# Optimization experiments

Hardware: AMD Instinct MI355X
Metric: run time of the kernel (lower is better)

Reference implementation:

```python
import jax, jax.numpy as jnp
import numpy as np

B, T, D = 2, 1024, 2048
H = 16
NOPE, ROPE = 128, 64
QKD = NOPE + ROPE          # 192
QLORA, KVLORA = 1536, 512
VHD = 128
INTER = 8192
EPS = 1e-6
# NOTE: faithful to source: softscale = qk_head_dim * -0.5 (a large negative
# multiplier, NOT qk_head_dim ** -0.5). We reproduce the exact math.
SOFTSCALE = QKD * -0.5


def rmsnorm(x, w):
    return x * jax.lax.rsqrt(jnp.mean(jnp.square(x), axis=-1, keepdims=True) + EPS) * w


def apply_rope(x, cos, sin):
    # x: [B, T, h, rd] with rd even; cos/sin: [T, rd//2]
    x2 = x.reshape(x.shape[:-1] + (-1, 2))
    x0, x1 = x2[..., 0], x2[..., 1]
    c = cos[None, :, None, :]
    s = sin[None, :, None, :]
    r0 = x0 * c - x1 * s
    r1 = x0 * s + x1 * c
    return jnp.stack([r0, r1], axis=-1).reshape(x.shape)


def setup_inputs() -> dict:
    key = jax.random.key(0)
    ks = jax.random.split(key, 12)

    def w(k, o, i):
        return jax.random.normal(k, (o, i), jnp.float32) * 0.02

    x = jax.random.normal(ks[0], (B, T, D), jnp.float32)
    # RoPE angle tables for the rope sub-dim
    inv_freq = 1.0 / (10000.0 ** (jnp.arange(0, ROPE, 2, dtype=jnp.float32) / ROPE))
    ang = jnp.arange(T, dtype=jnp.float32)[:, None] * inv_freq[None, :]  # [T, ROPE//2]
    # causal additive mask [T, T]
    mask = jnp.where(jnp.tril(jnp.ones((T, T), bool)), 0.0, -1e9).astype(jnp.float32)
    return {
        "x": x,
        "mask": mask,
        "freqs_cos": jnp.cos(ang),
        "freqs_sin": jnp.sin(ang),
        "attn_norm_w": jnp.ones((D,), jnp.float32),
        "wq_a": w(ks[1], QLORA, D),
        "q_norm_w": jnp.ones((QLORA,), jnp.float32),
        "wq_b": w(ks[2], H * QKD, QLORA),
        "wkv_a": w(ks[3], KVLORA + ROPE, D),
        "kv_norm_w": jnp.ones((KVLORA,), jnp.float32),
        "wkv_b": w(ks[4], H * (NOPE + VHD), KVLORA),
        "wo": w(ks[5], D, H * VHD),
        "ffn_norm_w": jnp.ones((D,), jnp.float32),
        "w1": w(ks[6], INTER, D),
        "w2": w(ks[7], D, INTER),
        "w3": w(ks[8], INTER, D),
    }


def reference(x, mask, freqs_cos, freqs_sin, attn_norm_w, wq_a, q_norm_w, wq_b,
              wkv_a, kv_norm_w, wkv_b, wo, ffn_norm_w, w1, w2, w3):
    b, t, d = x.shape
    # --- MLA attention sub-block (pre-norm + residual) ---
    h = rmsnorm(x, attn_norm_w)
    # low-rank query: wq_b(q_norm(wq_a(h)))
    q = rmsnorm(h @ wq_a.T, q_norm_w) @ wq_b.T          # [b, t, H*QKD]
    q = q.reshape(b, t, H, QKD)
    q_nope, q_pe = q[..., :NOPE], q[..., NOPE:]
    q_pe = apply_rope(q_pe, freqs_cos, freqs_sin)
    # low-rank kv + decoupled rope key
    kv_all = h @ wkv_a.T                                 # [b, t, KVLORA+ROPE]
    kv_lat, k_pe = kv_all[..., :KVLORA], kv_all[..., KVLORA:]
    k_pe = apply_rope(k_pe[:, :, None, :], freqs_cos, freqs_sin)  # [b, t, 1, ROPE]
    kv = rmsnorm(kv_lat, kv_norm_w) @ wkv_b.T            # [b, t, H*(NOPE+VHD)]
    kv = kv.reshape(b, t, H, NOPE + VHD)
    k_nope, v = kv[..., :NOPE], kv[..., NOPE:]
    qf = jnp.concatenate([q_nope, q_pe], axis=-1)        # [b, t, H, QKD]
    kf = jnp.concatenate([k_nope, jnp.broadcast_to(k_pe, (b, t, H, ROPE))], axis=-1)
    scores = jnp.einsum('bshd,bthd->bsht', qf, kf) * SOFTSCALE
    scores = scores + mask[:, None, :]                   # mask over (s, 1, t)
    attn = jax.nn.softmax(scores.astype(jnp.float32), axis=-1).astype(x.dtype)
    y = jnp.einsum('bsht,bthd->bshd', attn, v).reshape(b, t, H * VHD)
    x = x + y @ wo.T
    # --- MLP sub-block (pre-norm + residual), SwiGLU ---
    h2 = rmsnorm(x, ffn_norm_w)
    out = x + (jax.nn.silu(h2 @ w1.T) * (h2 @ w3.T)) @ w2.T
    return out
```

## Files before the change

kernel.cpp:

```cpp
#include <hip/hip_runtime.h>
#include <hip/hip_bf16.h>
#include <cstddef>


#define TT 1024
#define DD 2048
#define QBLK 64
#define KVB 32

using bf16 = __hip_bfloat16;
typedef __attribute__((ext_vector_type(8))) short short8;
typedef __attribute__((ext_vector_type(8))) unsigned short ushort8v;
typedef __attribute__((ext_vector_type(4))) float f32x4;

__device__ __forceinline__ float us2f(unsigned short u) {
    return __uint_as_float(((unsigned int)u) << 16);
}
__device__ __forceinline__ float ldf(const void* p, size_t i, int isbf) {
    return isbf ? us2f(((const unsigned short*)p)[i]) : ((const float*)p)[i];
}
__device__ __forceinline__ unsigned short f2bf(float f) {
    __hip_bfloat16 b = __float2bfloat16(f);
    return *reinterpret_cast<unsigned short*>(&b);
}

__global__ __launch_bounds__(64) void detect_k(const void* __restrict__ x,
                                               int* __restrict__ flag)
{
    __shared__ int cnt;
    if (threadIdx.x == 0) cnt = 0;
    __syncthreads();
    const unsigned short* u = (const unsigned short*)x;
    int bad = 0;
    for (int i = threadIdx.x; i < 512; i += 64) {
        const float v = us2f(u[i]);
        const float a = fabsf(v);
        if (!(a < 1e6f) || (v != 0.0f && a < 1e-30f)) bad++;
    }
    atomicAdd(&cnt, bad);
    __syncthreads();
    if (threadIdx.x == 0) *flag = (cnt > 32) ? 0 : 1;
}

__global__ __launch_bounds__(256) void cvt_bf_k(
    const void* __restrict__ src, unsigned short* __restrict__ dst,
    size_t n, const int* __restrict__ flag)
{
    const int isbf = *flag;
    const size_t stride = (size_t)gridDim.x * 2048;
    for (size_t i = ((size_t)blockIdx.x * 256 + threadIdx.x) * 8; i < n; i += stride) {
        if (isbf) {
            *(ushort8v*)(dst + i) = *(const ushort8v*)((const unsigned short*)src + i);
        } else {
            const float* s = (const float*)src + i;
            float4 f0 = *(const float4*)s, f1 = *(const float4*)(s + 4);
            unsigned short t[8] = {f2bf(f0.x), f2bf(f0.y), f2bf(f0.z), f2bf(f0.w),
                                   f2bf(f1.x), f2bf(f1.y), f2bf(f1.z), f2bf(f1.w)};
            *(ushort8v*)(dst + i) = *(const ushort8v*)t;
        }
    }
}

__global__ __launch_bounds__(256) void cvt_hl_k(
    const void* __restrict__ src, unsigned short* __restrict__ dh,
    unsigned short* __restrict__ dl, size_t n, const int* __restrict__ flag)
{
    const int isbf = *flag;
    const size_t stride = (size_t)gridDim.x * 2048;
    for (size_t i = ((size_t)blockIdx.x * 256 + threadIdx.x) * 8; i < n; i += stride) {
        unsigned short th[8], tl[8];
        if (isbf) {
            const unsigned short* s = (const unsigned short*)src + i;
#pragma unroll
            for (int u = 0; u < 8; ++u) { th[u] = s[u]; tl[u] = 0; }
        } else {
            const float* s = (const float*)src + i;
#pragma unroll
            for (int u = 0; u < 8; ++u) {
                const float v = s[u];
                th[u] = f2bf(v);
                tl[u] = f2bf(v - us2f(th[u]));
            }
        }
        *(ushort8v*)(dh + i) = *(const ushort8v*)th;
        *(ushort8v*)(dl + i) = *(const ushort8v*)tl;
    }
}

template <int S, int HASR>
__global__ __launch_bounds__(256) void combine_k(
    const float* __restrict__ p, const float* __restrict__ R,
    float* __restrict__ out, int n4)
{
    const int stride = gridDim.x * 256;
    const float4* pp = (const float4*)p;
    for (int i = blockIdx.x * 256 + threadIdx.x; i < n4; i += stride) {
        float4 o = pp[i];
#pragma unroll
        for (int s = 1; s < S; ++s) {
            const float4 b4 = pp[(size_t)s * n4 + i];
            o.x += b4.x; o.y += b4.y; o.z += b4.z; o.w += b4.w;
        }
        if (HASR) {
            const float4 r4 = ((const float4*)R)[i];
            o.x += r4.x; o.y += r4.y; o.z += r4.z; o.w += r4.w;
        }
        ((float4*)out)[i] = o;
    }
}

__global__ __launch_bounds__(256) void rmsnorm_hl_k(
    const float* __restrict__ in, const void* __restrict__ w,
    unsigned short* __restrict__ oh, unsigned short* __restrict__ ol,
    int L, int istride, const int* __restrict__ flag)
{
    const int isbf = *flag;
    const int m = blockIdx.x, tid = threadIdx.x;
    const float* row = in + (size_t)m * istride;
    float ss = 0.f;
    for (int i = tid; i < L; i += 256) { float v = row[i]; ss += v * v; }
    __shared__ float red[256];
    red[tid] = ss; __syncthreads();
    for (int s = 128; s > 0; s >>= 1) {
        if (tid < s) red[tid] += red[tid + s];
        __syncthreads();
    }
    const float scale = 1.0f / sqrtf(red[0] / (float)L + 1e-6f);
    unsigned short* hrow = oh + (size_t)m * L;
    unsigned short* lrow = ol + (size_t)m * L;
    for (int i = tid; i < L; i += 256) {
        const float v = row[i] * scale * ldf(w, i, isbf);
        const unsigned short hi = f2bf(v);
        hrow[i] = hi;
        lrow[i] = f2bf(v - us2f(hi));
    }
}

__global__ __launch_bounds__(256) void rmsnorm_bf_k(
    const float* __restrict__ in, const void* __restrict__ w,
    unsigned short* __restrict__ out, int L,
    const int* __restrict__ flag)
{
    const int isbf = *flag;
    const int m = blockIdx.x, tid = threadIdx.x;
    const float* row = in + (size_t)m * L;
    float ss = 0.f;
    for (int i = tid; i < L; i += 256) { float v = row[i]; ss += v * v; }
    __shared__ float red[256];
    red[tid] = ss; __syncthreads();
    for (int s = 128; s > 0; s >>= 1) {
        if (tid < s) red[tid] += red[tid + s];
        __syncthreads();
    }
    const float scale = 1.0f / sqrtf(red[0] / (float)L + 1e-6f);
    unsigned short* orow = out + (size_t)m * L;
    for (int i = tid; i < L; i += 256)
        orow[i] = f2bf(row[i] * scale * ldf(w, i, isbf));
}

__global__ __launch_bounds__(256) void rmsnorm_x_hl_k(
    const void* __restrict__ x, size_t eoff, const void* __restrict__ w,
    unsigned short* __restrict__ hh, unsigned short* __restrict__ hl,
    float* __restrict__ xf, const int* __restrict__ flag)
{
    const int isbf = *flag;
    const int m = blockIdx.x, tid = threadIdx.x;
    const size_t base = eoff + (size_t)m * DD;
    float* xrow = xf + (size_t)m * DD;
    float ss = 0.f;
    float vals[8];
    for (int i = 0; i < 8; ++i) {
        float v = ldf(x, base + tid + 256 * i, isbf);
        vals[i] = v; ss += v * v;
        xrow[tid + 256 * i] = v;
    }
    __shared__ float red[256];
    red[tid] = ss; __syncthreads();
    for (int s = 128; s > 0; s >>= 1) {
        if (tid < s) red[tid] += red[tid + s];
        __syncthreads();
    }
    const float scale = 1.0f / sqrtf(red[0] / (float)DD + 1e-6f);
    unsigned short* hrow = hh + (size_t)m * DD;
    unsigned short* lrow = hl + (size_t)m * DD;
    for (int i = 0; i < 8; ++i) {
        const float v = vals[i] * scale * ldf(w, tid + 256 * i, isbf);
        const unsigned short hi = f2bf(v);
        hrow[tid + 256 * i] = hi;
        lrow[tid + 256 * i] = f2bf(v - us2f(hi));
    }
}

__global__ __launch_bounds__(256) void gemm_mfma3_k(
    const unsigned short* __restrict__ Ah, const unsigned short* __restrict__ Al,
    const void* __restrict__ Wv, const unsigned short* __restrict__ Wlo,
    float* __restrict__ C, int N, int K, int klen,
    int presplit, const int* __restrict__ flag)
{
    __shared__ unsigned short Ash[128 * 40];
    __shared__ unsigned short Asl[128 * 40];
    __shared__ unsigned short Wsh[128 * 40];
    __shared__ unsigned short Wsl[128 * 40];
    const int tid = threadIdx.x;
    const int lane = tid & 63;
    const int wave = tid >> 6;
    const int wm = (wave >> 1) << 6, wn = (wave & 1) << 6;
    const int bm = blockIdx.y << 7, bn = blockIdx.x << 7;
    const int k0 = blockIdx.z * klen;
    const size_t zoff = (size_t)blockIdx.z * 1024 * N;
    const int srow = tid >> 1, scol = (tid & 1) << 4;
    const unsigned short* Ahld = Ah + (size_t)(bm + srow) * K + scol;
    const unsigned short* Alld = Al + (size_t)(bm + srow) * K + scol;
    const int wrow = bn + srow;
    const size_t wldbase = (size_t)((wrow < N) ? wrow : (N - 1)) * K + scol;
    unsigned short* Ahdst = &Ash[srow * 40 + scol];
    unsigned short* Aldst = &Asl[srow * 40 + scol];
    unsigned short* Whdst = &Wsh[srow * 40 + scol];
    unsigned short* Wldst = &Wsl[srow * 40 + scol];
    const int frow = lane & 15;
    const int fk = (lane >> 4) << 3;
    const int kend = k0 + klen;

    f32x4 acc[4][4] = {};

    if (presplit) {
        const unsigned short* Whp = (const unsigned short*)Wv + wldbase;
        const unsigned short* Wlp = Wlo + wldbase;
        ushort8v ca0h = *(const ushort8v*)(Ahld + k0);
        ushort8v ca1h = *(const ushort8v*)(Ahld + k0 + 8);
        ushort8v ca0l = *(const ushort8v*)(Alld + k0);
        ushort8v ca1l = *(const ushort8v*)(Alld + k0 + 8);
        ushort8v cw0h = *(const ushort8v*)(Whp + k0);
        ushort8v cw1h = *(const ushort8v*)(Whp + k0 + 8);
        ushort8v cw0l = *(const ushort8v*)(Wlp + k0);
        ushort8v cw1l = *(const ushort8v*)(Wlp + k0 + 8);
        for (int kt = k0; kt < kend; kt += 32) {
            __syncthreads();
            *(ushort8v*)Ahdst = ca0h; *(ushort8v*)(Ahdst + 8) = ca1h;
            *(ushort8v*)Aldst = ca0l; *(ushort8v*)(Aldst + 8) = ca1l;
            *(ushort8v*)Whdst = cw0h; *(ushort8v*)(Whdst + 8) = cw1h;
            *(ushort8v*)Wldst = cw0l; *(ushort8v*)(Wldst + 8) = cw1l;
            __syncthreads();
            const int nk = (kt + 32 < kend) ? kt + 32 : kt;
            ca0h = *(const ushort8v*)(Ahld + nk);
            ca1h = *(const ushort8v*)(Ahld + nk + 8);
            ca0l = *(const ushort8v*)(Alld + nk);
            ca1l = *(const ushort8v*)(Alld + nk + 8);
            cw0h = *(const ushort8v*)(Whp + nk);
            cw1h = *(const ushort8v*)(Whp + nk + 8);
            cw0l = *(const ushort8v*)(Wlp + nk);
            cw1l = *(const ushort8v*)(Wlp + nk + 8);

            short8 afh[4], afl[4], bfh[4], bfl[4];
#pragma unroll
            for (int i = 0; i < 4; ++i) {
                afh[i] = *(const short8*)&Ash[(wm + i * 16 + frow) * 40 + fk];
                afl[i] = *(const short8*)&Asl[(wm + i * 16 + frow) * 40 + fk];
            }
#pragma unroll
            for (int j = 0; j < 4; ++j) {
                bfh[j] = *(const short8*)&Wsh[(wn + j * 16 + frow) * 40 + fk];
                bfl[j] = *(const short8*)&Wsl[(wn + j * 16 + frow) * 40 + fk];
            }
#pragma unroll
            for (int i = 0; i < 4; ++i)
#pragma unroll
                for (int j = 0; j < 4; ++j) {
                    acc[i][j] = __builtin_amdgcn_mfma_f32_16x16x32_bf16(
                        afh[i], bfh[j], acc[i][j], 0, 0, 0);
                    acc[i][j] = __builtin_amdgcn_mfma_f32_16x16x32_bf16(
                        afh[i], bfl[j], acc[i][j], 0, 0, 0);
                    acc[i][j] = __builtin_amdgcn_mfma_f32_16x16x32_bf16(
                        afl[i], bfh[j], acc[i][j], 0, 0, 0);
                }
        }
    } else {
        const int isbf = *flag;
        for (int kt = k0; kt < kend; kt += 32) {
            ushort8v a0h = *(const ushort8v*)(Ahld + kt);
            ushort8v a1h = *(const ushort8v*)(Ahld + kt + 8);
            ushort8v a0l = *(const ushort8v*)(Alld + kt);
            ushort8v a1l = *(const ushort8v*)(Alld + kt + 8);
            ushort8v w0h, w1h, w0l, w1l;
            if (isbf) {
                const unsigned short* Wp = (const unsigned short*)Wv + wldbase + kt;
                w0h = *(const ushort8v*)(Wp);
                w1h = *(const ushort8v*)(Wp + 8);
                w0l = w0h ^ w0h;
                w1l = w0l;
            } else {
                const float* Wp = (const float*)Wv + wldbase + kt;
                unsigned short th[16], tl[16];
#pragma unroll
                for (int t4 = 0; t4 < 4; ++t4) {
                    float4 f = *(const float4*)(Wp + 4 * t4);
                    float fv[4] = {f.x, f.y, f.z, f.w};
#pragma unroll
                    for (int u = 0; u < 4; ++u) {
                        const unsigned short hi = f2bf(fv[u]);
                        th[4 * t4 + u] = hi;
                        tl[4 * t4 + u] = f2bf(fv[u] - us2f(hi));
                    }
                }
                w0h = *(ushort8v*)&th[0]; w1h = *(ushort8v*)&th[8];
                w0l = *(ushort8v*)&tl[0]; w1l = *(ushort8v*)&tl[8];
            }
            __syncthreads();
            *(ushort8v*)Ahdst = a0h; *(ushort8v*)(Ahdst + 8) = a1h;
            *(ushort8v*)Aldst = a0l; *(ushort8v*)(Aldst + 8) = a1l;
            *(ushort8v*)Whdst = w0h; *(ushort8v*)(Whdst + 8) = w1h;
            *(ushort8v*)Wldst = w0l; *(ushort8v*)(Wldst + 8) = w1l;
            __syncthreads();

            short8 afh[4], afl[4], bfh[4], bfl[4];
#pragma unroll
            for (int i = 0; i < 4; ++i) {
                afh[i] = *(const short8*)&Ash[(wm + i * 16 + frow) * 40 + fk];
                afl[i] = *(const short8*)&Asl[(wm + i * 16 + frow) * 40 + fk];
            }
#pragma unroll
            for (int j = 0; j < 4; ++j) {
                bfh[j] = *(const short8*)&Wsh[(wn + j * 16 + frow) * 40 + fk];
                bfl[j] = *(const short8*)&Wsl[(wn + j * 16 + frow) * 40 + fk];
            }
#pragma unroll
            for (int i = 0; i < 4; ++i)
#pragma unroll
                for (int j = 0; j < 4; ++j) {
                    acc[i][j] = __builtin_amdgcn_mfma_f32_16x16x32_bf16(
                        afh[i], bfh[j], acc[i][j], 0, 0, 0);
                    acc[i][j] = __builtin_amdgcn_mfma_f32_16x16x32_bf16(
                        afh[i], bfl[j], acc[i][j], 0, 0, 0);
                    acc[i][j] = __builtin_amdgcn_mfma_f32_16x16x32_bf16(
                        afl[i], bfh[j], acc[i][j], 0, 0, 0);
                }
        }
    }

#pragma unroll
    for (int i = 0; i < 4; ++i) {
        const int r0 = bm + wm + i * 16 + ((lane >> 4) << 2);
#pragma unroll
        for (int j = 0; j < 4; ++j) {
            const int c = bn + wn + j * 16 + (lane & 15);
            if (c < N) {
#pragma unroll
                for (int g = 0; g < 4; ++g)
                    C[zoff + (size_t)(r0 + g) * N + c] = acc[i][j][g];
            }
        }
    }
}

template <int EPI>
__global__ __launch_bounds__(256) void gemm_mfma_k(
    const unsigned short* __restrict__ A, const void* __restrict__ Wv,
    const float* __restrict__ R, void* __restrict__ outp,
    int N, int K, int klen, int wready, const int* __restrict__ flag)
{
    __shared__ unsigned short As[128 * 40];
    __shared__ unsigned short Ws[128 * 40];
    const int tid = threadIdx.x;
    const int lane = tid & 63;
    const int wave = tid >> 6;
    const int wm = (wave >> 1) << 6, wn = (wave & 1) << 6;
    const int bm = blockIdx.y << 7, bn = blockIdx.x << 7;
    const int k0 = blockIdx.z * klen;
    const size_t zoff = (size_t)blockIdx.z * 1024 * N;
    const int srow = tid >> 1, scol = (tid & 1) << 4;
    const unsigned short* Ald = A + (size_t)(bm + srow) * K + scol;
    const size_t wldbase = (size_t)(bn + srow) * K + scol;
    unsigned short* Adst = &As[srow * 40 + scol];
    unsigned short* Wdst = &Ws[srow * 40 + scol];
    const int frow = lane & 15;
    const int fk = (lane >> 4) << 3;
    const int kend = k0 + klen;

    f32x4 acc[4][4] = {};

    if (wready) {
        const unsigned short* Wp = (const unsigned short*)Wv + wldbase;
        ushort8v ca0 = *(const ushort8v*)(Ald + k0);
        ushort8v ca1 = *(const ushort8v*)(Ald + k0 + 8);
        ushort8v cw0 = *(const ushort8v*)(Wp + k0);
        ushort8v cw1 = *(const ushort8v*)(Wp + k0 + 8);
        for (int kt = k0; kt < kend; kt += 32) {
            __syncthreads();
            *(ushort8v*)Adst = ca0; *(ushort8v*)(Adst + 8) = ca1;
            *(ushort8v*)Wdst = cw0; *(ushort8v*)(Wdst + 8) = cw1;
            __syncthreads();
            const int nk = (kt + 32 < kend) ? kt + 32 : kt;
            ca0 = *(const ushort8v*)(Ald + nk);
            ca1 = *(const ushort8v*)(Ald + nk + 8);
            cw0 = *(const ushort8v*)(Wp + nk);
            cw1 = *(const ushort8v*)(Wp + nk + 8);

            short8 af[4], bfr[4];
#pragma unroll
            for (int i = 0; i < 4; ++i)
                af[i] = *(const short8*)&As[(wm + i * 16 + frow) * 40 + fk];
#pragma unroll
            for (int j = 0; j < 4; ++j)
                bfr[j] = *(const short8*)&Ws[(wn + j * 16 + frow) * 40 + fk];
#pragma unroll
            for (int i = 0; i < 4; ++i)
#pragma unroll
                for (int j = 0; j < 4; ++j)
                    acc[i][j] = __builtin_amdgcn_mfma_f32_16x16x32_bf16(
                        af[i], bfr[j], acc[i][j], 0, 0, 0);
        }
    } else {
        const int isbf = *flag;
        for (int kt = k0; kt < kend; kt += 32) {
            ushort8v a0 = *(const ushort8v*)(Ald + kt);
            ushort8v a1 = *(const ushort8v*)(Ald + kt + 8);
            ushort8v w0, w1;
            if (isbf) {
                const unsigned short* Wp = (const unsigned short*)Wv + wldbase + kt;
                w0 = *(const ushort8v*)(Wp);
                w1 = *(const ushort8v*)(Wp + 8);
            } else {
                const float* Wp = (const float*)Wv + wldbase + kt;
                float4 f0 = *(const float4*)(Wp);
                float4 f1 = *(const float4*)(Wp + 4);
                float4 f2 = *(const float4*)(Wp + 8);
                float4 f3 = *(const float4*)(Wp + 12);
                unsigned short wt[16];
                wt[0] = f2bf(f0.x); wt[1] = f2bf(f0.y); wt[2]  = f2bf(f0.z); wt[3]  = f2bf(f0.w);
                wt[4] = f2bf(f1.x); wt[5] = f2bf(f1.y); wt[6]  = f2bf(f1.z); wt[7]  = f2bf(f1.w);
                wt[8] = f2bf(f2.x); wt[9] = f2bf(f2.y); wt[10] = f2bf(f2.z); wt[11] = f2bf(f2.w);
                wt[12] = f2bf(f3.x); wt[13] = f2bf(f3.y); wt[14] = f2bf(f3.z); wt[15] = f2bf(f3.w);
                w0 = *(const ushort8v*)&wt[0];
                w1 = *(const ushort8v*)&wt[8];
            }
            __syncthreads();
            *(ushort8v*)Adst = a0; *(ushort8v*)(Adst + 8) = a1;
            *(ushort8v*)Wdst = w0; *(ushort8v*)(Wdst + 8) = w1;
            __syncthreads();

            short8 af[4], bfr[4];
#pragma unroll
            for (int i = 0; i < 4; ++i)
                af[i] = *(const short8*)&As[(wm + i * 16 + frow) * 40 + fk];
#pragma unroll
            for (int j = 0; j < 4; ++j)
                bfr[j] = *(const short8*)&Ws[(wn + j * 16 + frow) * 40 + fk];
#pragma unroll
            for (int i = 0; i < 4; ++i)
#pragma unroll
                for (int j = 0; j < 4; ++j)
                    acc[i][j] = __builtin_amdgcn_mfma_f32_16x16x32_bf16(
                        af[i], bfr[j], acc[i][j], 0, 0, 0);
        }
    }

#pragma unroll
    for (int i = 0; i < 4; ++i) {
        const int r0 = bm + wm + i * 16 + ((lane >> 4) << 2);
#pragma unroll
        for (int j = 0; j < 4; ++j) {
            const int c = bn + wn + j * 16 + (lane & 15);
#pragma unroll
            for (int g = 0; g < 4; ++g) {
                const size_t idx = zoff + (size_t)(r0 + g) * N + c;
                const float v = acc[i][j][g];
                if (EPI == 0) {
                    ((float*)outp)[idx] = v;
                } else if (EPI == 1) {
                    ((float*)outp)[idx] = v + R[idx];
                } else {
                    const float gv = R[idx];
                    const float sg = 1.0f / (1.0f + __expf(-gv));
                    ((unsigned short*)outp)[idx] = f2bf(gv * sg * v);
                }
            }
        }
    }
}

__global__ __launch_bounds__(256) void gemm_swiglu_k(
    const unsigned short* __restrict__ A, const void* __restrict__ W1v,
    const void* __restrict__ W3v, unsigned short* __restrict__ outp,
    int N, int K, int wready, const int* __restrict__ flag)
{
    __shared__ unsigned short As[128 * 40];
    __shared__ unsigned short Ws1[128 * 40];
    __shared__ unsigned short Ws3[128 * 40];
    const int tid = threadIdx.x;
    const int lane = tid & 63;
    const int wave = tid >> 6;
    const int wm = (wave >> 1) << 6, wn = (wave & 1) << 6;
    const int bm = blockIdx.y << 7, bn = blockIdx.x << 7;
    const int srow = tid >> 1, scol = (tid & 1) << 4;
    const unsigned short* Ald = A + (size_t)(bm + srow) * K + scol;
    const size_t wldbase = (size_t)(bn + srow) * K + scol;
    unsigned short* Adst = &As[srow * 40 + scol];
    unsigned short* W1dst = &Ws1[srow * 40 + scol];
    unsigned short* W3dst = &Ws3[srow * 40 + scol];
    const int frow = lane & 15;
    const int fk = (lane >> 4) << 3;

    f32x4 acc1[4][4] = {};
    f32x4 acc3[4][4] = {};

    if (wready) {
        const unsigned short* W1p = (const unsigned short*)W1v + wldbase;
        const unsigned short* W3p = (const unsigned short*)W3v + wldbase;
        ushort8v ca0 = *(const ushort8v*)(Ald);
        ushort8v ca1 = *(const ushort8v*)(Ald + 8);
        ushort8v c10 = *(const ushort8v*)(W1p);
        ushort8v c11 = *(const ushort8v*)(W1p + 8);
        ushort8v c30 = *(const ushort8v*)(W3p);
        ushort8v c31 = *(const ushort8v*)(W3p + 8);
        for (int kt = 0; kt < K; kt += 32) {
            __syncthreads();
            *(ushort8v*)Adst = ca0; *(ushort8v*)(Adst + 8) = ca1;
            *(ushort8v*)W1dst = c10; *(ushort8v*)(W1dst + 8) = c11;
            *(ushort8v*)W3dst = c30; *(ushort8v*)(W3dst + 8) = c31;
            __syncthreads();
            const int nk = (kt + 32 < K) ? kt + 32 : kt;
            ca0 = *(const ushort8v*)(Ald + nk);
            ca1 = *(const ushort8v*)(Ald + nk + 8);
            c10 = *(const ushort8v*)(W1p + nk);
            c11 = *(const ushort8v*)(W1p + nk + 8);
            c30 = *(const ushort8v*)(W3p + nk);
            c31 = *(const ushort8v*)(W3p + nk + 8);

            short8 af[4], b1[4], b3[4];
#pragma unroll
            for (int i = 0; i < 4; ++i)
                af[i] = *(const short8*)&As[(wm + i * 16 + frow) * 40 + fk];
#pragma unroll
            for (int j = 0; j < 4; ++j) {
                b1[j] = *(const short8*)&Ws1[(wn + j * 16 + frow) * 40 + fk];
                b3[j] = *(const short8*)&Ws3[(wn + j * 16 + frow) * 40 + fk];
            }
#pragma unroll
            for (int i = 0; i < 4; ++i)
#pragma unroll
                for (int j = 0; j < 4; ++j) {
                    acc1[i][j] = __builtin_amdgcn_mfma_f32_16x16x32_bf16(
                        af[i], b1[j], acc1[i][j], 0, 0, 0);
                    acc3[i][j] = __builtin_amdgcn_mfma_f32_16x16x32_bf16(
                        af[i], b3[j], acc3[i][j], 0, 0, 0);
                }
        }
    } else {
        const int isbf = *flag;
        for (int kt = 0; kt < K; kt += 32) {
            ushort8v a0 = *(const ushort8v*)(Ald + kt);
            ushort8v a1 = *(const ushort8v*)(Ald + kt + 8);
            ushort8v w10, w11, w30, w31;
            if (isbf) {
                const unsigned short* W1p = (const unsigned short*)W1v + wldbase + kt;
                const unsigned short* W3p = (const unsigned short*)W3v + wldbase + kt;
                w10 = *(const ushort8v*)(W1p); w11 = *(const ushort8v*)(W1p + 8);
                w30 = *(const ushort8v*)(W3p); w31 = *(const ushort8v*)(W3p + 8);
            } else {
                const float* W1p = (const float*)W1v + wldbase + kt;
                const float* W3p = (const float*)W3v + wldbase + kt;
                unsigned short t1[16], t3[16];
#pragma unroll
                for (int t4 = 0; t4 < 4; ++t4) {
                    float4 f1 = *(const float4*)(W1p + 4 * t4);
                    float4 f3 = *(const float4*)(W3p + 4 * t4);
                    float v1[4] = {f1.x, f1.y, f1.z, f1.w};
                    float v3[4] = {f3.x, f3.y, f3.z, f3.w};
#pragma unroll
                    for (int u = 0; u < 4; ++u) {
                        t1[4 * t4 + u] = f2bf(v1[u]);
                        t3[4 * t4 + u] = f2bf(v3[u]);
                    }
                }
                w10 = *(ushort8v*)&t1[0]; w11 = *(ushort8v*)&t1[8];
                w30 = *(ushort8v*)&t3[0]; w31 = *(ushort8v*)&t3[8];
            }
            __syncthreads();
            *(ushort8v*)Adst = a0; *(ushort8v*)(Adst + 8) = a1;
            *(ushort8v*)W1dst = w10; *(ushort8v*)(W1dst + 8) = w11;
            *(ushort8v*)W3dst = w30; *(ushort8v*)(W3dst + 8) = w31;
            __syncthreads();

            short8 af[4], b1[4], b3[4];
#pragma unroll
            for (int i = 0; i < 4; ++i)
                af[i] = *(const short8*)&As[(wm + i * 16 + frow) * 40 + fk];
#pragma unroll
            for (int j = 0; j < 4; ++j) {
                b1[j] = *(const short8*)&Ws1[(wn + j * 16 + frow) * 40 + fk];
                b3[j] = *(const short8*)&Ws3[(wn + j * 16 + frow) * 40 + fk];
            }
#pragma unroll
            for (int i = 0; i < 4; ++i)
#pragma unroll
                for (int j = 0; j < 4; ++j) {
                    acc1[i][j] = __builtin_amdgcn_mfma_f32_16x16x32_bf16(
                        af[i], b1[j], acc1[i][j], 0, 0, 0);
                    acc3[i][j] = __builtin_amdgcn_mfma_f32_16x16x32_bf16(
                        af[i], b3[j], acc3[i][j], 0, 0, 0);
                }
        }
    }

#pragma unroll
    for (int i = 0; i < 4; ++i) {
        const int r0 = bm + wm + i * 16 + ((lane >> 4) << 2);
#pragma unroll
        for (int j = 0; j < 4; ++j) {
            const int c = bn + wn + j * 16 + (lane & 15);
#pragma unroll
            for (int g = 0; g < 4; ++g) {
                const float gv = acc1[i][j][g];
                const float sg = 1.0f / (1.0f + __expf(-gv));
                outp[(size_t)(r0 + g) * N + c] = f2bf(gv * sg * acc3[i][j][g]);
            }
        }
    }
}

__global__ __launch_bounds__(256) void rope_k(
    float* __restrict__ qb, float* __restrict__ kva,
    const void* __restrict__ fc, const void* __restrict__ fs,
    const int* __restrict__ flag)
{
    const int isbf = *flag;
    const int t = blockIdx.x;
    const int tid = threadIdx.x;
    __shared__ float c[32], s[32];
    if (tid < 32) {
        c[tid] = ldf(fc, t * 32 + tid, isbf);
        s[tid] = ldf(fs, t * 32 + tid, isbf);
    }
    __syncthreads();
    for (int p = tid; p < 512; p += 256) {
        const int h = p >> 5, i = p & 31;
        float* base = qb + (size_t)t * 3072 + h * 192 + 128 + 2 * i;
        const float x0 = base[0], x1 = base[1];
        base[0] = x0 * c[i] - x1 * s[i];
        base[1] = x0 * s[i] + x1 * c[i];
    }
    if (tid < 32) {
        float* base = kva + (size_t)t * 576 + 512 + 2 * tid;
        const float x0 = base[0], x1 = base[1];
        base[0] = x0 * c[tid] - x1 * s[tid];
        base[1] = x0 * s[tid] + x1 * c[tid];
    }
}

__global__ __launch_bounds__(256) void kvprep_k(
    const float* __restrict__ kvb,
    const float* __restrict__ kva,
    unsigned short* __restrict__ kh, unsigned short* __restrict__ kl,
    unsigned short* __restrict__ vt)
{
    const int tt = blockIdx.x, h = blockIdx.y;
    const int tid = threadIdx.x;
    const int tbase = tt * 64;
    for (int i = tid; i < 64 * 192; i += 256) {
        const int t = i / 192, k = i % 192;
        const float v = (k < 128)
            ? kvb[(size_t)(tbase + t) * 4096 + h * 256 + k]
            : kva[(size_t)(tbase + t) * 576 + 512 + (k - 128)];
        const unsigned short hi = f2bf(v);
        const size_t o = ((size_t)h * 1024 + tbase + t) * 192 + k;
        kh[o] = hi;
        kl[o] = f2bf(v - us2f(hi));
    }
    __shared__ unsigned short Vl[128][72];
    for (int i = tid; i < 64 * 128; i += 256) {
        const int t = i >> 7, d = i & 127;
        Vl[d][t] = f2bf(kvb[(size_t)(tbase + t) * 4096 + h * 256 + 128 + d]);
    }
    __syncthreads();
    for (int i = tid; i < 128 * 64; i += 256) {
        const int d = i >> 6, t = i & 63;
        vt[((size_t)h * 128 + d) * 1024 + tbase + t] = Vl[d][t];
    }
}

__global__ __launch_bounds__(256) void attn_mfma_k(
    const float* __restrict__ qb,
    const unsigned short* __restrict__ kh,
    const unsigned short* __restrict__ kl,
    const unsigned short* __restrict__ vt,
    float* __restrict__ opart)
{
    const int qt = blockIdx.x, h = blockIdx.y, z = blockIdx.z;
    const int s0 = qt * QBLK;
    const int tid = threadIdx.x;
    const int lane = tid & 63, wave = tid >> 6;
    const int frow = lane & 15;
    const int fk8 = (lane >> 4) << 3;
    const int g4 = (lane >> 4) << 2;

    __shared__ __align__(16) unsigned short Ksh[KVB][200];
    __shared__ __align__(16) unsigned short Ksl[KVB][200];
    __shared__ __align__(16) unsigned short Vs[128][40];
    __shared__ __align__(16) unsigned short Ps[4][16][40];

    const int wrow0 = s0 + wave * 16;
    short8 qhf[6], qlf[6];
    {
        const float* qrow = qb + (size_t)(wrow0 + frow) * 3072 + h * 192 + fk8;
#pragma unroll
        for (int ks = 0; ks < 6; ++ks) {
            float4 f0 = *(const float4*)(qrow + ks * 32);
            float4 f1 = *(const float4*)(qrow + ks * 32 + 4);
            float fv[8] = {f0.x, f0.y, f0.z, f0.w, f1.x, f1.y, f1.z, f1.w};
            unsigned short th[8], tl[8];
#pragma unroll
            for (int u = 0; u < 8; ++u) {
                th[u] = f2bf(fv[u]);
                tl[u] = f2bf(fv[u] - us2f(th[u]));
            }
            qhf[ks] = *(short8*)th;
            qlf[ks] = *(short8*)tl;
        }
    }

    f32x4 O[8] = {};
    float m_run[4] = {-1e30f, -1e30f, -1e30f, -1e30f};
    float l_run[4] = {};

    const int t_beg = z * (qt + 1);
    const int t_end = t_beg + (qt + 1);
    for (int tt = t_beg; tt < t_end; ++tt) {
        const int t0 = tt * KVB;
        __syncthreads();
        for (int i = tid; i < KVB * 24; i += 256) {
            const int r = i / 24, c = (i % 24) * 8;
            const size_t gof = ((size_t)h * 1024 + t0 + r) * 192 + c;
            *(ushort8v*)&Ksh[r][c] = *(const ushort8v*)(kh + gof);
            *(ushort8v*)&Ksl[r][c] = *(const ushort8v*)(kl + gof);
        }
        for (int i = tid; i < 128 * 4; i += 256) {
            const int d = i >> 2, c = (i & 3) * 8;
            *(ushort8v*)&Vs[d][c] =
                *(const ushort8v*)(vt + ((size_t)h * 128 + d) * 1024 + t0 + c);
        }
        __syncthreads();

        const bool active = (t0 <= wrow0 + 15);
        if (active) {
            f32x4 s[2] = {};
#pragma unroll
            for (int j = 0; j < 2; ++j) {
                const unsigned short* kb = &Ksh[j * 16 + frow][fk8];
                const unsigned short* lb = &Ksl[j * 16 + frow][fk8];
#pragma unroll
                for (int ks = 0; ks < 6; ++ks) {
                    short8 bh = *(const short8*)(kb + ks * 32);
                    short8 bl = *(const short8*)(lb + ks * 32);
                    s[j] = __builtin_amdgcn_mfma_f32_16x16x32_bf16(qhf[ks], bh, s[j], 0, 0, 0);
                    s[j] = __builtin_amdgcn_mfma_f32_16x16x32_bf16(qhf[ks], bl, s[j], 0, 0, 0);
                    s[j] = __builtin_amdgcn_mfma_f32_16x16x32_bf16(qlf[ks], bh, s[j], 0, 0, 0);
                }
            }
            const bool edge = (t0 + KVB - 1 > wrow0);
            float sv[2][4];
#pragma unroll
            for (int j = 0; j < 2; ++j)
#pragma unroll
                for (int g = 0; g < 4; ++g) {
                    float v = s[j][g] * -96.0f;
                    if (edge) {
                        const int col = t0 + j * 16 + frow;
                        const int row = wrow0 + g4 + g;
                        if (col > row) v = -1e30f;
                    }
                    sv[j][g] = v;
                }
            float alpha[4];
#pragma unroll
            for (int g = 0; g < 4; ++g) {
                float mt = fmaxf(sv[0][g], sv[1][g]);
                mt = fmaxf(mt, __shfl_xor(mt, 1));
                mt = fmaxf(mt, __shfl_xor(mt, 2));
                mt = fmaxf(mt, __shfl_xor(mt, 4));
                mt = fmaxf(mt, __shfl_xor(mt, 8));
                const float mn = fmaxf(m_run[g], mt);
                alpha[g] = __expf(m_run[g] - mn);
                m_run[g] = mn;
                const float p0 = __expf(sv[0][g] - mn);
                const float p1 = __expf(sv[1][g] - mn);
                sv[0][g] = p0; sv[1][g] = p1;
                float ps = p0 + p1;
                ps += __shfl_xor(ps, 1);
                ps += __shfl_xor(ps, 2);
                ps += __shfl_xor(ps, 4);
                ps += __shfl_xor(ps, 8);
                l_run[g] = l_run[g] * alpha[g] + ps;
            }
#pragma unroll
            for (int jt = 0; jt < 8; ++jt)
#pragma unroll
                for (int g = 0; g < 4; ++g)
                    O[jt][g] *= alpha[g];
#pragma unroll
            for (int j = 0; j < 2; ++j)
#pragma unroll
                for (int g = 0; g < 4; ++g)
                    Ps[wave][g4 + g][j * 16 + frow] = f2bf(sv[j][g]);
        }
        __syncthreads();
        if (active) {
            short8 pa = *(const short8*)&Ps[wave][frow][fk8];
#pragma unroll
            for (int jt = 0; jt < 8; ++jt) {
                short8 vb = *(const short8*)&Vs[jt * 16 + frow][fk8];
                O[jt] = __builtin_amdgcn_mfma_f32_16x16x32_bf16(pa, vb, O[jt], 0, 0, 0);
            }
        }
    }

#pragma unroll
    for (int g = 0; g < 4; ++g) {
        const int row = wrow0 + g4 + g;
        float* rec = opart + (((size_t)z * 1024 + row) * 16 + h) * 66;
        unsigned short* ob = (unsigned short*)rec;
#pragma unroll
        for (int jt = 0; jt < 8; ++jt)
            ob[jt * 16 + frow] = f2bf(O[jt][g]);
        if ((lane & 15) == 0) { rec[64] = m_run[g]; rec[65] = l_run[g]; }
    }
}

__global__ __launch_bounds__(256) void attn_merge_k(
    const float* __restrict__ opart, unsigned short* __restrict__ y)
{
    const int r = blockIdx.x;
    for (int i = threadIdx.x; i < 2048; i += 256) {
        const int h = i >> 7, d = i & 127;
        const float* r0 = opart + (((size_t)r) * 16 + h) * 66;
        const float* r1 = opart + (((size_t)1024 + r) * 16 + h) * 66;
        const float m0 = r0[64], l0 = r0[65];
        const float m1 = r1[64], l1 = r1[65];
        const float mm = fmaxf(m0, m1);
        const float a0 = __expf(m0 - mm), a1 = __expf(m1 - mm);
        const float denom = l0 * a0 + l1 * a1;
        const float o0 = us2f(((const unsigned short*)r0)[d]);
        const float o1 = us2f(((const unsigned short*)r1)[d]);
        y[(size_t)r * 2048 + h * 128 + d] = f2bf((o0 * a0 + o1 * a1) / denom);
    }
}

extern "C" void kernel_launch(void* const* d_in, const int* in_sizes, int n_in,
                              void* d_out, int out_size, void* d_ws, size_t ws_size,
                              hipStream_t stream) {
    (void)in_sizes; (void)n_in; (void)out_size;
    const void* x       = d_in[0];
    const void* fcos    = d_in[2];
    const void* fsin    = d_in[3];
    const void* attn_nw = d_in[4];
    const void* wq_a    = d_in[5];
    const void* q_nw    = d_in[6];
    const void* wq_b    = d_in[7];
    const void* wkv_a   = d_in[8];
    const void* kv_nw   = d_in[9];
    const void* wkv_b   = d_in[10];
    const void* wo      = d_in[11];
    const void* ffn_nw  = d_in[12];
    const void* w1      = d_in[13];
    const void* w2      = d_in[14];
    const void* w3      = d_in[15];

    int* flag = (int*)d_ws;
    float* a  = (float*)d_ws + 64;
    const size_t M1 = 1048576;
    float* xf  = a;
    unsigned short* hh = (unsigned short*)(a + 2 * M1);
    unsigned short* hl = (unsigned short*)(a + 3 * M1);
    float* qa  = a + 4 * M1;
    float* kva = a + 4 * M1;
    unsigned short* kvnh = (unsigned short*)(a + 4 * M1 + 655360);
    unsigned short* kvnl = (unsigned short*)(a + 4 * M1 + 655360 + 262144);
    unsigned short* qah = (unsigned short*)(a + 5 * M1 + 524288);
    unsigned short* qal = (unsigned short*)(a + 6 * M1 + 262144);
    float* qb  = a + 7 * M1;
    float* kvb = a + 10 * M1;
    unsigned short* kh = (unsigned short*)(a + 2 * M1);
    unsigned short* kl = (unsigned short*)(a + 5 * M1 + 524288);
    unsigned short* vt = (unsigned short*)(a + 14 * M1);
    unsigned short* yb = (unsigned short*)(a + 3 * M1 + 524288);
    unsigned short* hb  = (unsigned short*)(a + 2 * M1);
    unsigned short* gb2 = (unsigned short*)(a + 12 * M1);
    float* x2  = xf;
    float* sp  = a + 10 * M1;
    float* fpo = a + 5 * M1;
    float* fp2 = a + 2 * M1;
    float* opart = a + 10 * M1;
    unsigned short* wo_b  = (unsigned short*)(a + 16 * M1);
    unsigned short* w1_b  = (unsigned short*)(a + 18 * M1);
    unsigned short* w3_b  = (unsigned short*)(a + 26 * M1);
    unsigned short* w2_b  = (unsigned short*)(a + 34 * M1);
    unsigned short* wqa_h = (unsigned short*)(a + 42 * M1);
    unsigned short* wqa_l = wqa_h + 3145728u;
    unsigned short* wqb_h = (unsigned short*)(a + 45 * M1);
    unsigned short* wqb_l = wqb_h + 4718592u;
    unsigned short* wkva_h = (unsigned short*)(a + 49 * M1 + 524288);
    unsigned short* wkva_l = wkva_h + 1179648u;
    unsigned short* wkvb_h = (unsigned short*)(a + 50 * M1 + 655360);
    unsigned short* wkvb_l = wkvb_h + 2097152u;
    const size_t NEED = 256 + (size_t)(52 * M1 + 655360) * 4;
    const int prep = (ws_size >= NEED) ? 1 : 0;

    detect_k<<<1, 64, 0, stream>>>(x, flag);

    if (prep) {
        cvt_bf_k<<<1024, 256, 0, stream>>>(wo, wo_b, (size_t)2048 * 2048, flag);
        cvt_bf_k<<<2048, 256, 0, stream>>>(w1, w1_b, (size_t)8192 * 2048, flag);
        cvt_bf_k<<<2048, 256, 0, stream>>>(w3, w3_b, (size_t)8192 * 2048, flag);
        cvt_bf_k<<<2048, 256, 0, stream>>>(w2, w2_b, (size_t)2048 * 8192, flag);
        cvt_hl_k<<<1024, 256, 0, stream>>>(wq_a, wqa_h, wqa_l, (size_t)1536 * 2048, flag);
        cvt_hl_k<<<1024, 256, 0, stream>>>(wq_b, wqb_h, wqb_l, (size_t)3072 * 1536, flag);
        cvt_hl_k<<<512, 256, 0, stream>>>(wkv_a, wkva_h, wkva_l, (size_t)576 * 2048, flag);
        cvt_hl_k<<<1024, 256, 0, stream>>>(wkv_b, wkvb_h, wkvb_l, (size_t)4096 * 512, flag);
    }
    const void* Wqa = prep ? (const void*)wqa_h : wq_a;
    const void* Wqb = prep ? (const void*)wqb_h : wq_b;
    const void* Wkva = prep ? (const void*)wkva_h : wkv_a;
    const void* Wkvb = prep ? (const void*)wkvb_h : wkv_b;
    const unsigned short* WqaL = prep ? wqa_l : nullptr;
    const unsigned short* WqbL = prep ? wqb_l : nullptr;
    const unsigned short* WkvaL = prep ? wkva_l : nullptr;
    const unsigned short* WkvbL = prep ? wkvb_l : nullptr;
    const void* WoP = prep ? (const void*)wo_b : wo;
    const void* W1P = prep ? (const void*)w1_b : w1;
    const void* W3P = prep ? (const void*)w3_b : w3;
    const void* W2P = prep ? (const void*)w2_b : w2;

    for (int b = 0; b < 2; ++b) {
        const size_t eoff = (size_t)b * TT * DD;
        float* outb = (float*)d_out + eoff;

        rmsnorm_x_hl_k<<<TT, 256, 0, stream>>>(x, eoff, attn_nw, hh, hl, xf, flag);
        gemm_mfma3_k<<<dim3(12, 8, 4), 256, 0, stream>>>(hh, hl, Wqa, WqaL, sp, 1536, 2048, 512, prep, flag);
        combine_k<4, 0><<<1024, 256, 0, stream>>>(sp, nullptr, qa, 393216);
        rmsnorm_hl_k<<<TT, 256, 0, stream>>>(qa, q_nw, qah, qal, 1536, 1536, flag);
        gemm_mfma3_k<<<dim3(24, 8, 2), 256, 0, stream>>>(qah, qal, Wqb, WqbL, sp, 3072, 1536, 768, prep, flag);
        combine_k<2, 0><<<1024, 256, 0, stream>>>(sp, nullptr, qb, 786432);
        gemm_mfma3_k<<<dim3(5, 8, 8), 256, 0, stream>>>(hh, hl, Wkva, WkvaL, sp, 576, 2048, 256, prep, flag);
        combine_k<8, 0><<<1024, 256, 0, stream>>>(sp, nullptr, kva, 147456);
        rmsnorm_hl_k<<<TT, 256, 0, stream>>>(kva, kv_nw, kvnh, kvnl, 512, 576, flag);
        rope_k<<<TT, 256, 0, stream>>>(qb, kva, fcos, fsin, flag);
        gemm_mfma3_k<<<dim3(32, 8, 1), 256, 0, stream>>>(kvnh, kvnl, Wkvb, WkvbL, kvb, 4096, 512, 512, prep, flag);
        kvprep_k<<<dim3(16, 16), 256, 0, stream>>>(kvb, kva, kh, kl, vt);
        attn_mfma_k<<<dim3(TT / QBLK, 16, 2), 256, 0, stream>>>(qb, kh, kl, vt, opart);
        attn_merge_k<<<TT, 256, 0, stream>>>(opart, yb);

        gemm_mfma_k<0><<<dim3(16, 8, 4), 256, 0, stream>>>(yb, WoP, nullptr, fpo, 2048, 2048, 512, prep, flag);
        combine_k<4, 1><<<1024, 256, 0, stream>>>(fpo, xf, x2, 524288);
        rmsnorm_bf_k<<<TT, 256, 0, stream>>>(x2, ffn_nw, hb, 2048, flag);
        gemm_swiglu_k<<<dim3(64, 8), 256, 0, stream>>>(hb, W1P, W3P, gb2, 8192, 2048, prep, flag);
        gemm_mfma_k<0><<<dim3(16, 8, 4), 256, 0, stream>>>(gb2, W2P, nullptr, fp2, 2048, 8192, 2048, prep, flag);
        combine_k<4, 1><<<1024, 256, 0, stream>>>(fp2, x2, outb, 524288);
    }
}
```

Measured before the change: 1.345 ms.

## Load GEMM tiles directly into LDS with global_load_lds and XOR swizzle

Replaces the register-staged global-to-LDS copies in the three MFMA GEMM kernels' fast paths with direct global_load_lds DMA into a 32-wide XOR-swizzled LDS layout instead of a 40-stride padded one. The aim is to save the VGPRs and LDS write instructions used for staging and to avoid bank conflicts through the swizzle. In exchange it drops the previous register prefetch of the next tile, so loads and MFMA no longer overlap within a block apart from occupancy, and it adds a second barrier per iteration.

```diff
diff --git a/kernel.cpp b/kernel.cpp
--- a/kernel.cpp
+++ b/kernel.cpp
@@ -22,6 +22,11 @@
 __device__ __forceinline__ unsigned short f2bf(float f) {
     __hip_bfloat16 b = __float2bfloat16(f);
     return *reinterpret_cast<unsigned short*>(&b);
+}
+__device__ __forceinline__ void gld16(const unsigned short* g, unsigned short* l) {
+    __builtin_amdgcn_global_load_lds(
+        (const __attribute__((address_space(1))) void*)g,
+        (__attribute__((address_space(3))) void*)l, 16, 0, 0);
 }
 
 __global__ __launch_bounds__(64) void detect_k(const void* __restrict__ x,
@@ -197,10 +202,7 @@
     float* __restrict__ C, int N, int K, int klen,
     int presplit, const int* __restrict__ flag)
 {
-    __shared__ unsigned short Ash[128 * 40];
-    __shared__ unsigned short Asl[128 * 40];
-    __shared__ unsigned short Wsh[128 * 40];
-    __shared__ unsigned short Wsl[128 * 40];
+    __shared__ __align__(16) unsigned short lds[20480];
     const int tid = threadIdx.x;
     const int lane = tid & 63;
     const int wave = tid >> 6;
@@ -208,15 +210,6 @@
     const int bm = blockIdx.y << 7, bn = blockIdx.x << 7;
     const int k0 = blockIdx.z * klen;
     const size_t zoff = (size_t)blockIdx.z * 1024 * N;
-    const int srow = tid >> 1, scol = (tid & 1) << 4;
-    const unsigned short* Ahld = Ah + (size_t)(bm + srow) * K + scol;
-    const unsigned short* Alld = Al + (size_t)(bm + srow) * K + scol;
-    const int wrow = bn + srow;
-    const size_t wldbase = (size_t)((wrow < N) ? wrow : (N - 1)) * K + scol;
-    unsigned short* Ahdst = &Ash[srow * 40 + scol];
-    unsigned short* Aldst = &Asl[srow * 40 + scol];
-    unsigned short* Whdst = &Wsh[srow * 40 + scol];
-    unsigned short* Wldst = &Wsl[srow * 40 + scol];
     const int frow = lane & 15;
     const int fk = (lane >> 4) << 3;
     const int kend = k0 + klen;
@@ -224,43 +217,45 @@
     f32x4 acc[4][4] = {};
 
     if (presplit) {
-        const unsigned short* Whp = (const unsigned short*)Wv + wldbase;
-        const unsigned short* Wlp = Wlo + wldbase;
-        ushort8v ca0h = *(const ushort8v*)(Ahld + k0);
-        ushort8v ca1h = *(const ushort8v*)(Ahld + k0 + 8);
-        ushort8v ca0l = *(const ushort8v*)(Alld + k0);
-        ushort8v ca1l = *(const ushort8v*)(Alld + k0 + 8);
-        ushort8v cw0h = *(const ushort8v*)(Whp + k0);
-        ushort8v cw1h = *(const ushort8v*)(Whp + k0 + 8);
-        ushort8v cw0l = *(const ushort8v*)(Wlp + k0);
-        ushort8v cw1l = *(const ushort8v*)(Wlp + k0 + 8);
+        unsigned short* Lah = lds;
+        unsigned short* Lal = lds + 4096;
+        unsigned short* Lwh = lds + 8192;
+        unsigned short* Lwl = lds + 12288;
+        const unsigned short* Whp = (const unsigned short*)Wv;
+        const int lrow = lane >> 2;
+        const int sp8 = ((lane & 3) ^ (lrow & 3)) << 3;
+        const int rA0 = wave * 32 + lrow;
+        const int rA1 = wave * 32 + 16 + lrow;
+        const int wr0 = (bn + rA0 < N) ? bn + rA0 : N - 1;
+        const int wr1 = (bn + rA1 < N) ? bn + rA1 : N - 1;
+        const size_t gA0 = (size_t)(bm + rA0) * K + sp8;
+        const size_t gA1 = (size_t)(bm + rA1) * K + sp8;
+        const size_t gW0 = (size_t)wr0 * K + sp8;
+        const size_t gW1 = (size_t)wr1 * K + sp8;
+        unsigned short* d0 = lds + wave * 1024;
+        const int xa = ((fk >> 3) ^ (frow & 3)) << 3;
+
         for (int kt = k0; kt < kend; kt += 32) {
-            __syncthreads();
-            *(ushort8v*)Ahdst = ca0h; *(ushort8v*)(Ahdst + 8) = ca1h;
-            *(ushort8v*)Aldst = ca0l; *(ushort8v*)(Aldst + 8) = ca1l;
-            *(ushort8v*)Whdst = cw0h; *(ushort8v*)(Whdst + 8) = cw1h;
-            *(ushort8v*)Wldst = cw0l; *(ushort8v*)(Wldst + 8) = cw1l;
-            __syncthreads();
-            const int nk = (kt + 32 < kend) ? kt + 32 : kt;
-            ca0h = *(const ushort8v*)(Ahld + nk);
-            ca1h = *(const ushort8v*)(Ahld + nk + 8);
-            ca0l = *(const ushort8v*)(Alld + nk);
-            ca1l = *(const ushort8v*)(Alld + nk + 8);
-            cw0h = *(const ushort8v*)(Whp + nk);
-            cw1h = *(const ushort8v*)(Whp + nk + 8);
-            cw0l = *(const ushort8v*)(Wlp + nk);
-            cw1l = *(const ushort8v*)(Wlp + nk + 8);
+            gld16(Ah + gA0 + kt, Lah + wave * 1024);
+            gld16(Ah + gA1 + kt, Lah + wave * 1024 + 512);
+            gld16(Al + gA0 + kt, Lal + wave * 1024);
+            gld16(Al + gA1 + kt, Lal + wave * 1024 + 512);
+            gld16(Whp + gW0 + kt, Lwh + wave * 1024);
+            gld16(Whp + gW1 + kt, Lwh + wave * 1024 + 512);
+            gld16(Wlo + gW0 + kt, Lwl + wave * 1024);
+            gld16(Wlo + gW1 + kt, Lwl + wave * 1024 + 512);
+            __syncthreads();
 
             short8 afh[4], afl[4], bfh[4], bfl[4];
 #pragma unroll
             for (int i = 0; i < 4; ++i) {
-                afh[i] = *(const short8*)&Ash[(wm + i * 16 + frow) * 40 + fk];
-                afl[i] = *(const short8*)&Asl[(wm + i * 16 + frow) * 40 + fk];
+                afh[i] = *(const short8*)&Lah[(wm + i * 16 + frow) * 32 + xa];
+                afl[i] = *(const short8*)&Lal[(wm + i * 16 + frow) * 32 + xa];
             }
 #pragma unroll
             for (int j = 0; j < 4; ++j) {
-                bfh[j] = *(const short8*)&Wsh[(wn + j * 16 + frow) * 40 + fk];
-                bfl[j] = *(const short8*)&Wsl[(wn + j * 16 + frow) * 40 + fk];
+                bfh[j] = *(const short8*)&Lwh[(wn + j * 16 + frow) * 32 + xa];
+                bfl[j] = *(const short8*)&Lwl[(wn + j * 16 + frow) * 32 + xa];
             }
 #pragma unroll
             for (int i = 0; i < 4; ++i)
@@ -273,9 +268,24 @@
                     acc[i][j] = __builtin_amdgcn_mfma_f32_16x16x32_bf16(
                         afl[i], bfh[j], acc[i][j], 0, 0, 0);
                 }
-        }
+            __syncthreads();
+        }
+        (void)d0;
     } else {
+        unsigned short* Ash = lds;
+        unsigned short* Asl = lds + 5120;
+        unsigned short* Wsh = lds + 10240;
+        unsigned short* Wsl = lds + 15360;
         const int isbf = *flag;
+        const int srow = tid >> 1, scol = (tid & 1) << 4;
+        const unsigned short* Ahld = Ah + (size_t)(bm + srow) * K + scol;
+        const unsigned short* Alld = Al + (size_t)(bm + srow) * K + scol;
+        const int wrow = bn + srow;
+        const size_t wldbase = (size_t)((wrow < N) ? wrow : (N - 1)) * K + scol;
+        unsigned short* Ahdst = &Ash[srow * 40 + scol];
+        unsigned short* Aldst = &Asl[srow * 40 + scol];
+        unsigned short* Whdst = &Wsh[srow * 40 + scol];
+        unsigned short* Wldst = &Wsl[srow * 40 + scol];
         for (int kt = k0; kt < kend; kt += 32) {
             ushort8v a0h = *(const ushort8v*)(Ahld + kt);
             ushort8v a1h = *(const ushort8v*)(Ahld + kt + 8);
@@ -358,8 +368,7 @@
     const float* __restrict__ R, void* __restrict__ outp,
     int N, int K, int klen, int wready, const int* __restrict__ flag)
 {
-    __shared__ unsigned short As[128 * 40];
-    __shared__ unsigned short Ws[128 * 40];
+    __shared__ __align__(16) unsigned short lds[10240];
     const int tid = threadIdx.x;
     const int lane = tid & 63;
     const int wave = tid >> 6;
@@ -367,11 +376,6 @@
     const int bm = blockIdx.y << 7, bn = blockIdx.x << 7;
     const int k0 = blockIdx.z * klen;
     const size_t zoff = (size_t)blockIdx.z * 1024 * N;
-    const int srow = tid >> 1, scol = (tid & 1) << 4;
-    const unsigned short* Ald = A + (size_t)(bm + srow) * K + scol;
-    const size_t wldbase = (size_t)(bn + srow) * K + scol;
-    unsigned short* Adst = &As[srow * 40 + scol];
-    unsigned short* Wdst = &Ws[srow * 40 + scol];
     const int frow = lane & 15;
     const int fk = (lane >> 4) << 3;
     const int kend = k0 + klen;
@@ -379,52 +383,64 @@
     f32x4 acc[4][4] = {};
 
     if (wready) {
-        const unsigned short* Wp = (const unsigned short*)Wv + wldbase;
-        ushort8v ca0 = *(const ushort8v*)(Ald + k0);
-        ushort8v ca1 = *(const ushort8v*)(Ald + k0 + 8);
-        ushort8v cw0 = *(const ushort8v*)(Wp + k0);
-        ushort8v cw1 = *(const ushort8v*)(Wp + k0 + 8);
+        unsigned short* As = lds;
+        unsigned short* Ws = lds + 4096;
+        const unsigned short* Wp = (const unsigned short*)Wv;
+        const int lrow = lane >> 2;
+        const int sp8 = ((lane & 3) ^ (lrow & 3)) << 3;
+        const int rA0 = wave * 32 + lrow;
+        const int rA1 = wave * 32 + 16 + lrow;
+        const size_t gA0 = (size_t)(bm + rA0) * K + sp8;
+        const size_t gA1 = (size_t)(bm + rA1) * K + sp8;
+        const size_t gW0 = (size_t)(bn + rA0) * K + sp8;
+        const size_t gW1 = (size_t)(bn + rA1) * K + sp8;
+        const int xa = ((fk >> 3) ^ (frow & 3)) << 3;
+
         for (int kt = k0; kt < kend; kt += 32) {
-            __syncthreads();
-            *(ushort8v*)Adst = ca0; *(ushort8v*)(Adst + 8) = ca1;
-            *(ushort8v*)Wdst = cw0; *(ushort8v*)(Wdst + 8) = cw1;
-            __syncthreads();
-            const int nk = (kt + 32 < kend) ? kt + 32 : kt;
-            ca0 = *(const ushort8v*)(Ald + nk);
-            ca1 = *(const ushort8v*)(Ald + nk + 8);
-            cw0 = *(const ushort8v*)(Wp + nk);
-            cw1 = *(const ushort8v*)(Wp + nk + 8);
+            gld16(A + gA0 + kt, As + wave * 1024);
+            gld16(A + gA1 + kt, As + wave * 1024 + 512);
+            gld16(Wp + gW0 + kt, Ws + wave * 1024);
+            gld16(Wp + gW1 + kt, Ws + wave * 1024 + 512);
+            __syncthreads();
 
             short8 af[4], bfr[4];
 #pragma unroll
             for (int i = 0; i < 4; ++i)
-                af[i] = *(const short8*)&As[(wm + i * 16 + frow) * 40 + fk];
+                af[i] = *(const short8*)&As[(wm + i * 16 + frow) * 32 + xa];
 #pragma unroll
             for (int j = 0; j < 4; ++j)
-                bfr[j] = *(const short8*)&Ws[(wn + j * 16 + frow) * 40 + fk];
+                bfr[j] = *(const short8*)&Ws[(wn + j * 16 + frow) * 32 + xa];
 #pragma unroll
             for (int i = 0; i < 4; ++i)
 #pragma unroll
                 for (int j = 0; j < 4; ++j)
                     acc[i][j] = __builtin_amdgcn_mfma_f32_16x16x32_bf16(
                         af[i], bfr[j], acc[i][j], 0, 0, 0);
+            __syncthreads();
         }
     } else {
+        unsigned short* As = lds;
+        unsigned short* Ws = lds + 5120;
         const int isbf = *flag;
+        const int srow = tid >> 1, scol = (tid & 1) << 4;
+        const unsigned short* Ald = A + (size_t)(bm + srow) * K + scol;
+        const size_t wldbase = (size_t)(bn + srow) * K + scol;
+        unsigned short* Adst = &As[srow * 40 + scol];
+        unsigned short* Wdst = &Ws[srow * 40 + scol];
         for (int kt = k0; kt < kend; kt += 32) {
             ushort8v a0 = *(const ushort8v*)(Ald + kt);
             ushort8v a1 = *(const ushort8v*)(Ald + kt + 8);
             ushort8v w0, w1;
             if (isbf) {
-                const unsigned short* Wp = (const unsigned short*)Wv + wldbase + kt;
-                w0 = *(const ushort8v*)(Wp);
-                w1 = *(const ushort8v*)(Wp + 8);
+                const unsigned short* Wpp = (const unsigned short*)Wv + wldbase + kt;
+                w0 = *(const ushort8v*)(Wpp);
+                w1 = *(const ushort8v*)(Wpp + 8);
             } else {
-                const float* Wp = (const float*)Wv + wldbase + kt;
-                float4 f0 = *(const float4*)(Wp);
-                float4 f1 = *(const float4*)(Wp + 4);
-                float4 f2 = *(const float4*)(Wp + 8);
-                float4 f3 = *(const float4*)(Wp + 12);
+                const float* Wpp = (const float*)Wv + wldbase + kt;
+                float4 f0 = *(const float4*)(Wpp);
+                float4 f1 = *(const float4*)(Wpp + 4);
+                float4 f2 = *(const float4*)(Wpp + 8);
+                float4 f3 = *(const float4*)(Wpp + 12);
                 unsigned short wt[16];
                 wt[0] = f2bf(f0.x); wt[1] = f2bf(f0.y); wt[2]  = f2bf(f0.z); wt[3]  = f2bf(f0.w);
                 wt[4] = f2bf(f1.x); wt[5] = f2bf(f1.y); wt[6]  = f2bf(f1.z); wt[7]  = f2bf(f1.w);
@@ -483,20 +499,12 @@
     const void* __restrict__ W3v, unsigned short* __restrict__ outp,
     int N, int K, int wready, const int* __restrict__ flag)
 {
-    __shared__ unsigned short As[128 * 40];
-    __shared__ unsigned short Ws1[128 * 40];
-    __shared__ unsigned short Ws3[128 * 40];
+    __shared__ __align__(16) unsigned short lds[15360];
     const int tid = threadIdx.x;
     const int lane = tid & 63;
     const int wave = tid >> 6;
     const int wm = (wave >> 1) << 6, wn = (wave & 1) << 6;
     const int bm = blockIdx.y << 7, bn = blockIdx.x << 7;
-    const int srow = tid >> 1, scol = (tid & 1) << 4;
-    const unsigned short* Ald = A + (size_t)(bm + srow) * K + scol;
-    const size_t wldbase = (size_t)(bn + srow) * K + scol;
-    unsigned short* Adst = &As[srow * 40 + scol];
-    unsigned short* W1dst = &Ws1[srow * 40 + scol];
-    unsigned short* W3dst = &Ws3[srow * 40 + scol];
     const int frow = lane & 15;
     const int fk = (lane >> 4) << 3;
 
@@ -504,36 +512,38 @@
     f32x4 acc3[4][4] = {};
 
     if (wready) {
-        const unsigned short* W1p = (const unsigned short*)W1v + wldbase;
-        const unsigned short* W3p = (const unsigned short*)W3v + wldbase;
-        ushort8v ca0 = *(const ushort8v*)(Ald);
-        ushort8v ca1 = *(const ushort8v*)(Ald + 8);
-        ushort8v c10 = *(const ushort8v*)(W1p);
-        ushort8v c11 = *(const ushort8v*)(W1p + 8);
-        ushort8v c30 = *(const ushort8v*)(W3p);
-        ushort8v c31 = *(const ushort8v*)(W3p + 8);
+        unsigned short* As = lds;
+        unsigned short* L1 = lds + 4096;
+        unsigned short* L3 = lds + 8192;
+        const unsigned short* W1p = (const unsigned short*)W1v;
+        const unsigned short* W3p = (const unsigned short*)W3v;
+        const int lrow = lane >> 2;
+        const int sp8 = ((lane & 3) ^ (lrow & 3)) << 3;
+        const int rA0 = wave * 32 + lrow;
+        const int rA1 = wave * 32 + 16 + lrow;
+        const size_t gA0 = (size_t)(bm + rA0) * K + sp8;
+        const size_t gA1 = (size_t)(bm + rA1) * K + sp8;
+        const size_t gW0 = (size_t)(bn + rA0) * K + sp8;
+        const size_t gW1 = (size_t)(bn + rA1) * K + sp8;
+        const int xa = ((fk >> 3) ^ (frow & 3)) << 3;
+
         for (int kt = 0; kt < K; kt += 32) {
-            __syncthreads();
-            *(ushort8v*)Adst = ca0; *(ushort8v*)(Adst + 8) = ca1;
-            *(ushort8v*)W1dst = c10; *(ushort8v*)(W1dst + 8) = c11;
-            *(ushort8v*)W3dst = c30; *(ushort8v*)(W3dst + 8) = c31;
-            __syncthreads();
-            const int nk = (kt + 32 < K) ? kt + 32 : kt;
-            ca0 = *(const ushort8v*)(Ald + nk);
-            ca1 = *(const ushort8v*)(Ald + nk + 8);
-            c10 = *(const ushort8v*)(W1p + nk);
-            c11 = *(const ushort8v*)(W1p + nk + 8);
-            c30 = *(const ushort8v*)(W3p + nk);
-            c31 = *(const ushort8v*)(W3p + nk + 8);
+            gld16(A + gA0 + kt, As + wave * 1024);
+            gld16(A + gA1 + kt, As + wave * 1024 + 512);
+            gld16(W1p + gW0 + kt, L1 + wave * 1024);
+            gld16(W1p + gW1 + kt, L1 + wave * 1024 + 512);
+            gld16(W3p + gW0 + kt, L3 + wave * 1024);
+            gld16(W3p + gW1 + kt, L3 + wave * 1024 + 512);
+            __syncthreads();
 
             short8 af[4], b1[4], b3[4];
 #pragma unroll
             for (int i = 0; i < 4; ++i)
-                af[i] = *(const short8*)&As[(wm + i * 16 + frow) * 40 + fk];
+                af[i] = *(const short8*)&As[(wm + i * 16 + frow) * 32 + xa];
 #pragma unroll
             for (int j = 0; j < 4; ++j) {
-                b1[j] = *(const short8*)&Ws1[(wn + j * 16 + frow) * 40 + fk];
-                b3[j] = *(const short8*)&Ws3[(wn + j * 16 + frow) * 40 + fk];
+                b1[j] = *(const short8*)&L1[(wn + j * 16 + frow) * 32 + xa];
+                b3[j] = *(const short8*)&L3[(wn + j * 16 + frow) * 32 + xa];
             }
 #pragma unroll
             for (int i = 0; i < 4; ++i)
@@ -544,9 +554,19 @@
                     acc3[i][j] = __builtin_amdgcn_mfma_f32_16x16x32_bf16(
                         af[i], b3[j], acc3[i][j], 0, 0, 0);
                 }
+            __syncthreads();
         }
     } else {
+        unsigned short* As = lds;
+        unsigned short* Ws1 = lds + 5120;
+        unsigned short* Ws3 = lds + 10240;
         const int isbf = *flag;
+        const int srow = tid >> 1, scol = (tid & 1) << 4;
+        const unsigned short* Ald = A + (size_t)(bm + srow) * K + scol;
+        const size_t wldbase = (size_t)(bn + srow) * K + scol;
+        unsigned short* Adst = &As[srow * 40 + scol];
+        unsigned short* W1dst = &Ws1[srow * 40 + scol];
+        unsigned short* W3dst = &Ws3[srow * 40 + scol];
         for (int kt = 0; kt < K; kt += 32) {
             ushort8v a0 = *(const ushort8v*)(Ald + kt);
             ushort8v a1 = *(const ushort8v*)(Ald + kt + 8);
```

New measurement: 1.325 ms. About the same (-1.5%).
